# Kernel tuning notes

Measured on AMD Instinct MI355X. Metric: run time of the kernel, lower is better.

The kernel has to match this reference:

```python
import jax, jax.numpy as jnp
import numpy as np

HEADS = 16
DIM = 1024
D_K = DIM // HEADS
SEQ = 2048


def setup_inputs() -> dict:
    key = jax.random.key(0)
    ks = jax.random.split(key, 11)
    s = 1.0 / np.sqrt(DIM).astype(np.float32)
    return {
        "q": jax.random.normal(ks[0], (SEQ, DIM), jnp.float32),
        "k": jax.random.normal(ks[1], (SEQ, DIM), jnp.float32),
        "v": jax.random.normal(ks[2], (SEQ, DIM), jnp.float32),
        "Wq": jax.random.normal(ks[3], (DIM, DIM), jnp.float32) * s,
        "bq": jax.random.normal(ks[4], (DIM,), jnp.float32) * 0.01,
        "Wk": jax.random.normal(ks[5], (DIM, DIM), jnp.float32) * s,
        "bk": jax.random.normal(ks[6], (DIM,), jnp.float32) * 0.01,
        "Wv": jax.random.normal(ks[7], (DIM, DIM), jnp.float32) * s,
        "bv": jax.random.normal(ks[8], (DIM,), jnp.float32) * 0.01,
        "Wo": jax.random.normal(ks[9], (DIM, DIM), jnp.float32) * s,
        "bo": jax.random.normal(ks[10], (DIM,), jnp.float32) * 0.01,
    }


def reference(q, k, v, Wq, bq, Wk, bk, Wv, bv, Wo, bo):
    S = q.shape[0]
    # torch Linear: x @ W.T + b; view to (1, S, H, d_k) then transpose to (1, H, S, d_k)
    def proj(x, W, b):
        return (x @ W.T + b).reshape(1, S, HEADS, D_K).transpose(0, 2, 1, 3)

    qh = proj(q, Wq, bq)  # (1, H, S, d)
    kh = proj(k, Wk, bk)
    vh = proj(v, Wv, bv)

    scale = 1.0 / np.sqrt(D_K).astype(np.float32)
    scores = jnp.einsum("bhqd,bhkd->bhqk", qh, kh) * scale  # (1, H, S, S)
    # NOTE: source applies softmax over dim=1 == the HEADS axis (faithful quirk)
    attn = jax.nn.softmax(scores, axis=1)
    ctx = jnp.einsum("bhqk,bhkd->bhqd", attn, vh)  # (1, H, S, d)
    concat = ctx.transpose(0, 2, 1, 3).reshape(1, S, DIM)
    return concat @ Wo.T + bo
```

## Files before the change

kernel.cpp:

```cpp
#include <hip/hip_runtime.h>
#include <hip/hip_fp16.h>


typedef _Float16 f16;
typedef _Float16 f16x4 __attribute__((ext_vector_type(4)));
typedef _Float16 f16x8 __attribute__((ext_vector_type(8)));
typedef float    f32x4 __attribute__((ext_vector_type(4)));

#define S_LEN 2048
#define DIM   1024
#define NH    16
#define DK    64
#define EXP2K 0.1803368801111244f

#define MFMA(a, b, c) __builtin_amdgcn_mfma_f32_16x16x32_f16(a, b, c, 0, 0, 0)

#define VM_WAIT0   asm volatile("s_waitcnt vmcnt(0)" ::: "memory")
#define WG_BARRIER asm volatile("s_barrier" ::: "memory")

typedef __attribute__((address_space(1))) void g_void;
typedef __attribute__((address_space(3))) void l_void;

static __device__ __forceinline__ void gload_lds16(const void* g, void* l) {
  __builtin_amdgcn_global_load_lds((g_void*)g, (l_void*)l, 16, 0, 0);
}

static __device__ __forceinline__ float exp_s(float s) {
  return __builtin_amdgcn_exp2f(s * EXP2K);
}

__global__ __launch_bounds__(256) void cvt_all(
    const float* __restrict__ q, const float* __restrict__ k, const float* __restrict__ v,
    const float* __restrict__ Wq, const float* __restrict__ Wk, const float* __restrict__ Wv,
    const float* __restrict__ Wo, f16* __restrict__ qh, f16* __restrict__ kh,
    f16* __restrict__ vh, f16* __restrict__ wqh, f16* __restrict__ wkh,
    f16* __restrict__ wvh, f16* __restrict__ woh) {
  const size_t M = 1048576;
  const int seg = blockIdx.y;
  const float* src;
  f16* dst;
  switch (seg) {
    case 0: src = q;      dst = qh;      break;
    case 1: src = q + M;  dst = qh + M;  break;
    case 2: src = k;      dst = kh;      break;
    case 3: src = k + M;  dst = kh + M;  break;
    case 4: src = v;      dst = vh;      break;
    case 5: src = v + M;  dst = vh + M;  break;
    case 6: src = Wq;     dst = wqh;     break;
    case 7: src = Wk;     dst = wkh;     break;
    case 8: src = Wv;     dst = wvh;     break;
    default: src = Wo;    dst = woh;     break;
  }
  int i = blockIdx.x * 256 + threadIdx.x;
  float4 vv = ((const float4*)src)[i];
  f16x4 o = {(f16)vv.x, (f16)vv.y, (f16)vv.z, (f16)vv.w};
  ((f16x4*)dst)[i] = o;
}

__global__ __launch_bounds__(256) void sum_halves(const f16* __restrict__ a,
                                                  const f16* __restrict__ b,
                                                  f16* __restrict__ o) {
  int i = blockIdx.x * 256 + threadIdx.x;
  f16x8 x = ((const f16x8*)a)[i];
  f16x8 y = ((const f16x8*)b)[i];
  f16x8 r;
#pragma unroll
  for (int j = 0; j < 8; j++) r[j] = (f16)((float)x[j] + (float)y[j]);
  ((f16x8*)o)[i] = r;
}

static __device__ __forceinline__ void gemm32_core(const f16* __restrict__ X,
                                                   const f16* __restrict__ W,
                                                   int k0, int k1, int bm, int bn,
                                                   f16* As, f16* Bs,
                                                   f32x4 (&acc)[4][2]) {
  const int tid = threadIdx.x;
  const int wv = tid >> 6;
  const int lane = tid & 63;
  const int qd = lane >> 4;
  const int l16 = lane & 15;
  const int wm = (wv & 1) * 64;
  const int wn = (wv >> 1) * 32;
  const int lr4 = lane >> 2, lc4 = lane & 3;

  const f16* gA = X + (size_t)(bm + wv * 32 + lr4) * DIM + k0 + lc4 * 8;
  const f16* gB = W + (size_t)(bn + wv * 16 + lr4) * DIM + k0 + lc4 * 8;
  const int np = (k1 - k0) >> 5;

  gload_lds16(gA, As + (wv * 32) * 32);
  gload_lds16(gA + 16 * DIM, As + (wv * 32 + 16) * 32);
  gload_lds16(gB, Bs + (wv * 16) * 32);

#pragma unroll 2
  for (int t = 0; t < np; t++) {
    const int buf = t & 1;
    VM_WAIT0;
    WG_BARRIER;
    if (t + 1 < np) {
      const f16* gA1 = gA + (t + 1) * 32;
      const f16* gB1 = gB + (t + 1) * 32;
      f16* dA = As + (buf ^ 1) * (128 * 32);
      f16* dB = Bs + (buf ^ 1) * (64 * 32);
      gload_lds16(gA1, dA + (wv * 32) * 32);
      gload_lds16(gA1 + 16 * DIM, dA + (wv * 32 + 16) * 32);
      gload_lds16(gB1, dB + (wv * 16) * 32);
    }
    const f16* A = As + buf * (128 * 32);
    const f16* B = Bs + buf * (64 * 32);
    f16x8 bf[2];
#pragma unroll
    for (int ni = 0; ni < 2; ni++)
      bf[ni] = *(const f16x8*)&B[(wn + ni * 16 + l16) * 32 + qd * 8];
#pragma unroll
    for (int mi = 0; mi < 4; mi++) {
      f16x8 af = *(const f16x8*)&A[(wm + mi * 16 + l16) * 32 + qd * 8];
#pragma unroll
      for (int ni = 0; ni < 2; ni++)
        acc[mi][ni] = MFMA(af, bf[ni], acc[mi][ni]);
    }
  }
}

__global__ __launch_bounds__(256) void gemm_qkv(
    const f16* __restrict__ X0, const f16* __restrict__ X1, const f16* __restrict__ X2,
    const f16* __restrict__ W0, const f16* __restrict__ W1, const f16* __restrict__ W2,
    const float* __restrict__ b0, const float* __restrict__ b1, const float* __restrict__ b2,
    f16* __restrict__ o0, f16* __restrict__ o1, f16* __restrict__ o2) {
  __shared__ __align__(16) f16 As[2 * 128 * 32];
  __shared__ __align__(16) f16 Bs[2 * 64 * 32];
  const int z = blockIdx.z;
  const f16* X = z == 0 ? X0 : z == 1 ? X1 : X2;
  const f16* W = z == 0 ? W0 : z == 1 ? W1 : W2;
  const float* bias = z == 0 ? b0 : z == 1 ? b1 : b2;
  f16* outh = z == 0 ? o0 : z == 1 ? o1 : o2;

  const int bm = blockIdx.y * 128, bn = blockIdx.x * 64;
  f32x4 acc[4][2];
#pragma unroll
  for (int a = 0; a < 4; a++)
#pragma unroll
    for (int b = 0; b < 2; b++) acc[a][b] = (f32x4){0.f, 0.f, 0.f, 0.f};

  gemm32_core(X, W, 0, DIM, bm, bn, As, Bs, acc);

  const int tid = threadIdx.x;
  const int wv = tid >> 6, lane = tid & 63;
  const int qd = lane >> 4, l16 = lane & 15;
  const int wm = (wv & 1) * 64, wn = (wv >> 1) * 32;
#pragma unroll
  for (int mi = 0; mi < 4; mi++) {
#pragma unroll
    for (int ni = 0; ni < 2; ni++) {
      const int gm = bm + wm + mi * 16 + qd * 4;
      const int gn = bn + wn + ni * 16 + l16;
      const float bs = bias[gn];
      if (z == 2) {
        f16x4 o = {(f16)(acc[mi][ni][0] + bs), (f16)(acc[mi][ni][1] + bs),
                   (f16)(acc[mi][ni][2] + bs), (f16)(acc[mi][ni][3] + bs)};
        const int pj = (gm & ~31) + ((gm >> 2) & 3) * 8 + ((gm >> 4) & 1) * 4;
        *(f16x4*)&outh[(size_t)gn * S_LEN + pj] = o;
      } else {
#pragma unroll
        for (int r = 0; r < 4; r++)
          outh[(size_t)(gm + r) * DIM + gn] = (f16)(acc[mi][ni][r] + bs);
      }
    }
  }
}

__global__ __launch_bounds__(256) void gemm_out(const f16* __restrict__ X,
                                                const f16* __restrict__ W,
                                                const float* __restrict__ bias,
                                                float* __restrict__ outf) {
  __shared__ __align__(16) f16 As[2 * 64 * 32];
  __shared__ __align__(16) f16 Bs[2 * 64 * 32];
  const int tid = threadIdx.x;
  const int wv = tid >> 6;
  const int lane = tid & 63;
  const int qd = lane >> 4;
  const int l16 = lane & 15;
  const int wm = (wv & 1) * 32;
  const int wn = (wv >> 1) * 32;
  const int lr4 = lane >> 2, lc4 = lane & 3;
  const int bm = blockIdx.y * 64, bn = blockIdx.x * 64;

  const f16* gA = X + (size_t)(bm + wv * 16 + lr4) * DIM + lc4 * 8;
  const f16* gB = W + (size_t)(bn + wv * 16 + lr4) * DIM + lc4 * 8;

  f32x4 acc[2][2];
#pragma unroll
  for (int a = 0; a < 2; a++)
#pragma unroll
    for (int b = 0; b < 2; b++) acc[a][b] = (f32x4){0.f, 0.f, 0.f, 0.f};

  gload_lds16(gA, As + (wv * 16) * 32);
  gload_lds16(gB, Bs + (wv * 16) * 32);

#pragma unroll 2
  for (int t = 0; t < 32; t++) {
    const int buf = t & 1;
    VM_WAIT0;
    WG_BARRIER;
    if (t + 1 < 32) {
      gload_lds16(gA + (t + 1) * 32, As + (buf ^ 1) * (64 * 32) + (wv * 16) * 32);
      gload_lds16(gB + (t + 1) * 32, Bs + (buf ^ 1) * (64 * 32) + (wv * 16) * 32);
    }
    const f16* A = As + buf * (64 * 32);
    const f16* B = Bs + buf * (64 * 32);
    f16x8 bf[2];
#pragma unroll
    for (int ni = 0; ni < 2; ni++)
      bf[ni] = *(const f16x8*)&B[(wn + ni * 16 + l16) * 32 + qd * 8];
#pragma unroll
    for (int mi = 0; mi < 2; mi++) {
      f16x8 af = *(const f16x8*)&A[(wm + mi * 16 + l16) * 32 + qd * 8];
#pragma unroll
      for (int ni = 0; ni < 2; ni++)
        acc[mi][ni] = MFMA(af, bf[ni], acc[mi][ni]);
    }
  }

#pragma unroll
  for (int mi = 0; mi < 2; mi++) {
#pragma unroll
    for (int ni = 0; ni < 2; ni++) {
      const int gm = bm + wm + mi * 16 + qd * 4;
      const int gn = bn + wn + ni * 16 + l16;
      const float bs = bias[gn];
#pragma unroll
      for (int r = 0; r < 4; r++)
        outf[(size_t)(gm + r) * DIM + gn] = acc[mi][ni][r] + bs;
    }
  }
}

__global__ __launch_bounds__(256) void attn_denom(const f16* __restrict__ Qp,
                                                  const f16* __restrict__ Kp,
                                                  f16* __restrict__ IDn) {
  __shared__ __align__(16) f16 Qs[2][2][64 * 32];
  __shared__ __align__(16) f16 Ks[2][2][64 * 32];
  const int tid = threadIdx.x;
  const int wv = tid >> 6;
  const int lane = tid & 63;
  const int qd = lane >> 4;
  const int l16 = lane & 15;
  const int wm = (wv & 1) * 32, wn = (wv >> 1) * 32;
  const int flat = blockIdx.x + (blockIdx.y << 5);
  const int nf = ((flat & 7) << 7) + (flat >> 3);
  const int bi = (nf >> 5) * 64, bj = (nf & 31) * 64;
  const int lr4 = lane >> 2, lc4 = lane & 3;
  const int kkw = wv & 1;
  const int q0 = (wv >> 1) * 2;
  const int ssw = (lc4 ^ ((lr4 >> 1) & 3)) * 8;
  const int rsw = (qd ^ ((l16 >> 1) & 3)) * 8;

  f32x4 dsum[2][2];
#pragma unroll
  for (int a = 0; a < 2; a++)
#pragma unroll
    for (int b = 0; b < 2; b++) dsum[a][b] = (f32x4){0.f, 0.f, 0.f, 0.f};

  {
    const f16* gq = Qp + (size_t)(bi + q0 * 16 + lr4) * DIM + kkw * 32 + ssw;
    const f16* gk = Kp + (size_t)(bj + q0 * 16 + lr4) * DIM + kkw * 32 + ssw;
#pragma unroll
    for (int t = 0; t < 2; t++) {
      gload_lds16(gq + (size_t)t * 16 * DIM, &Qs[0][kkw][(q0 + t) * 16 * 32]);
      gload_lds16(gk + (size_t)t * 16 * DIM, &Ks[0][kkw][(q0 + t) * 16 * 32]);
    }
  }

#pragma unroll 2
  for (int h = 0; h < NH; h++) {
    const int buf = h & 1;
    VM_WAIT0;
    WG_BARRIER;
    if (h + 1 < NH) {
      const f16* gq = Qp + (size_t)(bi + q0 * 16 + lr4) * DIM + (h + 1) * DK + kkw * 32 + ssw;
      const f16* gk = Kp + (size_t)(bj + q0 * 16 + lr4) * DIM + (h + 1) * DK + kkw * 32 + ssw;
#pragma unroll
      for (int t = 0; t < 2; t++) {
        gload_lds16(gq + (size_t)t * 16 * DIM, &Qs[buf ^ 1][kkw][(q0 + t) * 16 * 32]);
        gload_lds16(gk + (size_t)t * 16 * DIM, &Ks[buf ^ 1][kkw][(q0 + t) * 16 * 32]);
      }
    }

#pragma unroll
    for (int mi = 0; mi < 2; mi++) {
      f16x8 af0 = *(const f16x8*)&Qs[buf][0][(wm + mi * 16 + l16) * 32 + rsw];
      f16x8 af1 = *(const f16x8*)&Qs[buf][1][(wm + mi * 16 + l16) * 32 + rsw];
#pragma unroll
      for (int ni = 0; ni < 2; ni++) {
        f16x8 bf0 = *(const f16x8*)&Ks[buf][0][(wn + ni * 16 + l16) * 32 + rsw];
        f16x8 bf1 = *(const f16x8*)&Ks[buf][1][(wn + ni * 16 + l16) * 32 + rsw];
        f32x4 s = {0.f, 0.f, 0.f, 0.f};
        s = MFMA(af0, bf0, s);
        s = MFMA(af1, bf1, s);
#pragma unroll
        for (int r = 0; r < 4; r++) dsum[mi][ni][r] += exp_s(s[r]);
      }
    }
  }
#pragma unroll
  for (int mi = 0; mi < 2; mi++)
#pragma unroll
    for (int ni = 0; ni < 2; ni++)
#pragma unroll
      for (int r = 0; r < 4; r++) {
        const int gi = bi + wm + mi * 16 + qd * 4 + r;
        const int gj = bj + wn + ni * 16 + l16;
        const int pj = (gj & ~31) + ((gj >> 2) & 3) * 8 + ((gj >> 4) & 1) * 4 + (gj & 3);
        IDn[(size_t)gi * S_LEN + pj] = (f16)(1.f / dsum[mi][ni][r]);
      }
}

__global__ __launch_bounds__(256, 4) void attn_ctx(const f16* __restrict__ Qp,
                                                   const f16* __restrict__ Kp,
                                                   const f16* __restrict__ Vt,
                                                   const f16* __restrict__ IDn,
                                                   f16* __restrict__ C0,
                                                   f16* __restrict__ C1) {
  __shared__ __align__(16) f16 Ks[2][2][64 * 32];
  __shared__ __align__(16) f16 Vs[2][64 * 64];
  const int tid = threadIdx.x;
  const int wv = tid >> 6;
  const int lane = tid & 63;
  const int qd = lane >> 4;
  const int l16 = lane & 15;
  const int flat = blockIdx.x + (blockIdx.y << 5) + (blockIdx.z << 9);
  const int nf = ((flat & 7) << 7) + (flat >> 3);
  const int h = (nf >> 5) & 15;
  const int iw = (nf & 31) * 64 + wv * 16;
  const int z = nf >> 9;
  const int jb = z * 1024;
  f16* Cz = z == 0 ? C0 : C1;
  const int lr4 = lane >> 2, lc4 = lane & 3;
  const int lr8 = lane >> 3, lc8 = lane & 7;
  const int kkw = wv & 1;
  const int rhw = wv >> 1;
  const int ssw = (lc4 ^ ((lr4 >> 1) & 3)) * 8;
  const int rsw = (qd ^ ((l16 >> 1) & 3)) * 8;
  const int l7 = l16 & 7;

  f16x8 aq[2];
#pragma unroll
  for (int kk = 0; kk < 2; kk++)
    aq[kk] = *(const f16x8*)(Qp + (size_t)(iw + l16) * DIM + h * DK + kk * 32 + qd * 8);

  f32x4 acc[4];
#pragma unroll
  for (int b = 0; b < 4; b++) acc[b] = (f32x4){0.f, 0.f, 0.f, 0.f};

  f16x8 idn[2][2];

  auto issue = [&](int tt, int pb) {
    const int j1 = jb + tt * 64;
    const f16* gk = Kp + (size_t)(j1 + rhw * 16 + lr4) * DIM + h * DK + kkw * 32 + ssw;
    gload_lds16(gk, &Ks[pb][kkw][(rhw * 16) * 32]);
    gload_lds16(gk + (size_t)32 * DIM, &Ks[pb][kkw][(rhw * 16 + 32) * 32]);
    const f16* gv = Vt + (size_t)(h * DK + wv * 16 + lr8) * S_LEN + j1 + (lc8 ^ lr8) * 8;
    gload_lds16(gv, &Vs[pb][(wv * 16) * 64]);
    gload_lds16(gv + (size_t)8 * S_LEN, &Vs[pb][(wv * 16 + 8) * 64]);
#pragma unroll
    for (int js = 0; js < 2; js++)
      idn[pb][js] = *(const f16x8*)(IDn + (size_t)(iw + l16) * S_LEN + j1 + js * 32 + qd * 8);
  };

  issue(0, 0);

#pragma unroll 2
  for (int t = 0; t < 16; t++) {
    const int buf = t & 1;
    VM_WAIT0;
    WG_BARRIER;
    if (t + 1 < 16) issue(t + 1, buf ^ 1);

    f16x8 pa[2];
#pragma unroll
    for (int js = 0; js < 2; js++) {
      f16x8 bk0[2], bk1[2];
#pragma unroll
      for (int kk = 0; kk < 2; kk++) {
        bk0[kk] = *(const f16x8*)&Ks[buf][kk][((js * 2) * 16 + l16) * 32 + rsw];
        bk1[kk] = *(const f16x8*)&Ks[buf][kk][((js * 2 + 1) * 16 + l16) * 32 + rsw];
      }
      f32x4 st0 = {0.f, 0.f, 0.f, 0.f};
      f32x4 st1 = {0.f, 0.f, 0.f, 0.f};
      st0 = MFMA(bk0[0], aq[0], st0);
      st0 = MFMA(bk0[1], aq[1], st0);
      st1 = MFMA(bk1[0], aq[0], st1);
      st1 = MFMA(bk1[1], aq[1], st1);
      f16x8 p;
#pragma unroll
      for (int r = 0; r < 4; r++) p[r] = (f16)(exp_s(st0[r]) * (float)idn[buf][js][r]);
#pragma unroll
      for (int r = 0; r < 4; r++) p[4 + r] = (f16)(exp_s(st1[r]) * (float)idn[buf][js][4 + r]);
      pa[js] = p;
    }

#pragma unroll
    for (int js = 0; js < 2; js++) {
#pragma unroll
      for (int nd = 0; nd < 4; nd++) {
        f16x8 bv = *(const f16x8*)&Vs[buf][(nd * 16 + l16) * 64 +
                                          (((js * 4 + qd) ^ l7) * 8)];
        acc[nd] = MFMA(pa[js], bv, acc[nd]);
      }
    }
  }

#pragma unroll
  for (int nd = 0; nd < 4; nd++)
#pragma unroll
    for (int r = 0; r < 4; r++)
      Cz[(size_t)(iw + qd * 4 + r) * DIM + h * DK + nd * 16 + l16] = (f16)acc[nd][r];
}

extern "C" void kernel_launch(void* const* d_in, const int* in_sizes, int n_in,
                              void* d_out, int out_size, void* d_ws, size_t ws_size,
                              hipStream_t stream) {
  const float* q  = (const float*)d_in[0];
  const float* k  = (const float*)d_in[1];
  const float* v  = (const float*)d_in[2];
  const float* Wq = (const float*)d_in[3];
  const float* bq = (const float*)d_in[4];
  const float* Wk = (const float*)d_in[5];
  const float* bk = (const float*)d_in[6];
  const float* Wv = (const float*)d_in[7];
  const float* bv = (const float*)d_in[8];
  const float* Wo = (const float*)d_in[9];
  const float* bo = (const float*)d_in[10];
  float* out = (float*)d_out;

  f16* w = (f16*)d_ws;
  f16* qh  = w;
  f16* kh  = qh + (size_t)S_LEN * DIM;
  f16* vh  = kh + (size_t)S_LEN * DIM;
  f16* wqh = vh + (size_t)S_LEN * DIM;
  f16* wkh = wqh + (size_t)DIM * DIM;
  f16* wvh = wkh + (size_t)DIM * DIM;
  f16* woh = wvh + (size_t)DIM * DIM;
  f16* Qp  = woh + (size_t)DIM * DIM;
  f16* Kp  = Qp + (size_t)S_LEN * DIM;
  f16* Vt  = Kp + (size_t)S_LEN * DIM;
  f16* IDn = qh;
  f16* C0  = vh;
  f16* C1  = wqh;
  f16* Ct  = qh;

  dim3 b256(256);
  cvt_all<<<dim3(1024, 10), b256, 0, stream>>>(q, k, v, Wq, Wk, Wv, Wo,
                                               qh, kh, vh, wqh, wkh, wvh, woh);

  gemm_qkv<<<dim3(DIM / 64, S_LEN / 128, 3), b256, 0, stream>>>(
      qh, kh, vh, wqh, wkh, wvh, bq, bk, bv, Qp, Kp, Vt);

  attn_denom<<<dim3(S_LEN / 64, S_LEN / 64), b256, 0, stream>>>(Qp, Kp, IDn);
  attn_ctx<<<dim3(S_LEN / 64, NH, 2), b256, 0, stream>>>(Qp, Kp, Vt, IDn, C0, C1);

  const int n8 = S_LEN * DIM / 8;
  sum_halves<<<n8 / 256, b256, 0, stream>>>(C0, C1, Ct);

  gemm_out<<<dim3(DIM / 64, S_LEN / 64), b256, 0, stream>>>(Ct, woh, bo, out);
}
```

Baseline: 205.2 us.

## Fuse context half-sum into output GEMM and use K=64 swizzled LDS tiles

Removes the separate sum_halves kernel: the output GEMM now loads both context halves into registers, adds them, and writes the sum to LDS itself. Both GEMMs move from K-step 32 to K-step 64 with an XOR-swizzled LDS layout to avoid bank conflicts, halving the number of barrier iterations. Costs are double the LDS per block, which may lower occupancy, and register-staged A loads in gemm_out instead of direct global-to-LDS copies.

```diff
diff --git a/kernel.cpp b/kernel.cpp
--- a/kernel.cpp
+++ b/kernel.cpp
@@ -16,6 +16,7 @@
 #define MFMA(a, b, c) __builtin_amdgcn_mfma_f32_16x16x32_f16(a, b, c, 0, 0, 0)
 
 #define VM_WAIT0   asm volatile("s_waitcnt vmcnt(0)" ::: "memory")
+#define LGKM_WAIT0 asm volatile("s_waitcnt lgkmcnt(0)" ::: "memory")
 #define WG_BARRIER asm volatile("s_barrier" ::: "memory")
 
 typedef __attribute__((address_space(1))) void g_void;
@@ -57,21 +58,9 @@
   ((f16x4*)dst)[i] = o;
 }
 
-__global__ __launch_bounds__(256) void sum_halves(const f16* __restrict__ a,
-                                                  const f16* __restrict__ b,
-                                                  f16* __restrict__ o) {
-  int i = blockIdx.x * 256 + threadIdx.x;
-  f16x8 x = ((const f16x8*)a)[i];
-  f16x8 y = ((const f16x8*)b)[i];
-  f16x8 r;
-#pragma unroll
-  for (int j = 0; j < 8; j++) r[j] = (f16)((float)x[j] + (float)y[j]);
-  ((f16x8*)o)[i] = r;
-}
-
-static __device__ __forceinline__ void gemm32_core(const f16* __restrict__ X,
+static __device__ __forceinline__ void gemm64_core(const f16* __restrict__ X,
                                                    const f16* __restrict__ W,
-                                                   int k0, int k1, int bm, int bn,
+                                                   int bm, int bn,
                                                    f16* As, f16* Bs,
                                                    f32x4 (&acc)[4][2]) {
   const int tid = threadIdx.x;
@@ -81,42 +70,46 @@
   const int l16 = lane & 15;
   const int wm = (wv & 1) * 64;
   const int wn = (wv >> 1) * 32;
-  const int lr4 = lane >> 2, lc4 = lane & 3;
-
-  const f16* gA = X + (size_t)(bm + wv * 32 + lr4) * DIM + k0 + lc4 * 8;
-  const f16* gB = W + (size_t)(bn + wv * 16 + lr4) * DIM + k0 + lc4 * 8;
-  const int np = (k1 - k0) >> 5;
-
-  gload_lds16(gA, As + (wv * 32) * 32);
-  gload_lds16(gA + 16 * DIM, As + (wv * 32 + 16) * 32);
-  gload_lds16(gB, Bs + (wv * 16) * 32);
+  const int lr8 = lane >> 3, lc8 = lane & 7;
+  const int l7 = l16 & 7;
+
+  const f16* gA = X + (size_t)(bm + wv * 32 + lr8) * DIM + (lc8 ^ lr8) * 8;
+  const f16* gB = W + (size_t)(bn + wv * 16 + lr8) * DIM + (lc8 ^ lr8) * 8;
+
+  auto issue = [&](int t, f16* dA, f16* dB) {
+#pragma unroll
+    for (int g = 0; g < 4; g++)
+      gload_lds16(gA + (size_t)(g * 8) * DIM + t * 64, dA + (wv * 32 + g * 8) * 64);
+#pragma unroll
+    for (int g = 0; g < 2; g++)
+      gload_lds16(gB + (size_t)(g * 8) * DIM + t * 64, dB + (wv * 16 + g * 8) * 64);
+  };
+
+  issue(0, As, Bs);
 
 #pragma unroll 2
-  for (int t = 0; t < np; t++) {
+  for (int t = 0; t < 16; t++) {
     const int buf = t & 1;
     VM_WAIT0;
     WG_BARRIER;
-    if (t + 1 < np) {
-      const f16* gA1 = gA + (t + 1) * 32;
-      const f16* gB1 = gB + (t + 1) * 32;
-      f16* dA = As + (buf ^ 1) * (128 * 32);
-      f16* dB = Bs + (buf ^ 1) * (64 * 32);
-      gload_lds16(gA1, dA + (wv * 32) * 32);
-      gload_lds16(gA1 + 16 * DIM, dA + (wv * 32 + 16) * 32);
-      gload_lds16(gB1, dB + (wv * 16) * 32);
-    }
-    const f16* A = As + buf * (128 * 32);
-    const f16* B = Bs + buf * (64 * 32);
-    f16x8 bf[2];
-#pragma unroll
-    for (int ni = 0; ni < 2; ni++)
-      bf[ni] = *(const f16x8*)&B[(wn + ni * 16 + l16) * 32 + qd * 8];
-#pragma unroll
-    for (int mi = 0; mi < 4; mi++) {
-      f16x8 af = *(const f16x8*)&A[(wm + mi * 16 + l16) * 32 + qd * 8];
+    if (t + 1 < 16)
+      issue(t + 1, As + (buf ^ 1) * (128 * 64), Bs + (buf ^ 1) * (64 * 64));
+    const f16* A = As + buf * (128 * 64);
+    const f16* B = Bs + buf * (64 * 64);
+#pragma unroll
+    for (int kk = 0; kk < 2; kk++) {
+      const int slot = ((kk * 4 + qd) ^ l7) * 8;
+      f16x8 bf[2];
 #pragma unroll
       for (int ni = 0; ni < 2; ni++)
-        acc[mi][ni] = MFMA(af, bf[ni], acc[mi][ni]);
+        bf[ni] = *(const f16x8*)&B[(wn + ni * 16 + l16) * 64 + slot];
+#pragma unroll
+      for (int mi = 0; mi < 4; mi++) {
+        f16x8 af = *(const f16x8*)&A[(wm + mi * 16 + l16) * 64 + slot];
+#pragma unroll
+        for (int ni = 0; ni < 2; ni++)
+          acc[mi][ni] = MFMA(af, bf[ni], acc[mi][ni]);
+      }
     }
   }
 }
@@ -126,8 +119,8 @@
     const f16* __restrict__ W0, const f16* __restrict__ W1, const f16* __restrict__ W2,
     const float* __restrict__ b0, const float* __restrict__ b1, const float* __restrict__ b2,
     f16* __restrict__ o0, f16* __restrict__ o1, f16* __restrict__ o2) {
-  __shared__ __align__(16) f16 As[2 * 128 * 32];
-  __shared__ __align__(16) f16 Bs[2 * 64 * 32];
+  __shared__ __align__(16) f16 As[2 * 128 * 64];
+  __shared__ __align__(16) f16 Bs[2 * 64 * 64];
   const int z = blockIdx.z;
   const f16* X = z == 0 ? X0 : z == 1 ? X1 : X2;
   const f16* W = z == 0 ? W0 : z == 1 ? W1 : W2;
@@ -141,7 +134,7 @@
 #pragma unroll
     for (int b = 0; b < 2; b++) acc[a][b] = (f32x4){0.f, 0.f, 0.f, 0.f};
 
-  gemm32_core(X, W, 0, DIM, bm, bn, As, Bs, acc);
+  gemm64_core(X, W, bm, bn, As, Bs, acc);
 
   const int tid = threadIdx.x;
   const int wv = tid >> 6, lane = tid & 63;
@@ -168,12 +161,13 @@
   }
 }
 
-__global__ __launch_bounds__(256) void gemm_out(const f16* __restrict__ X,
+__global__ __launch_bounds__(256) void gemm_out(const f16* __restrict__ C0,
+                                                const f16* __restrict__ C1,
                                                 const f16* __restrict__ W,
                                                 const float* __restrict__ bias,
                                                 float* __restrict__ outf) {
-  __shared__ __align__(16) f16 As[2 * 64 * 32];
-  __shared__ __align__(16) f16 Bs[2 * 64 * 32];
+  __shared__ __align__(16) f16 As[2 * 64 * 64];
+  __shared__ __align__(16) f16 Bs[2 * 64 * 64];
   const int tid = threadIdx.x;
   const int wv = tid >> 6;
   const int lane = tid & 63;
@@ -181,11 +175,27 @@
   const int l16 = lane & 15;
   const int wm = (wv & 1) * 32;
   const int wn = (wv >> 1) * 32;
-  const int lr4 = lane >> 2, lc4 = lane & 3;
+  const int lr8 = lane >> 3, lc8 = lane & 7;
+  const int l7 = l16 & 7;
   const int bm = blockIdx.y * 64, bn = blockIdx.x * 64;
 
-  const f16* gA = X + (size_t)(bm + wv * 16 + lr4) * DIM + lc4 * 8;
-  const f16* gB = W + (size_t)(bn + wv * 16 + lr4) * DIM + lc4 * 8;
+  const f16* gA0 = C0 + (size_t)(bm + wv * 16 + lr8) * DIM + lc8 * 8;
+  const f16* gA1 = C1 + (size_t)(bm + wv * 16 + lr8) * DIM + lc8 * 8;
+  const f16* gB  = W + (size_t)(bn + wv * 16 + lr8) * DIM + (lc8 ^ lr8) * 8;
+
+  f16x8 a0[2], a1[2];
+  auto issueA = [&](int t) {
+#pragma unroll
+    for (int g = 0; g < 2; g++) {
+      a0[g] = *(const f16x8*)(gA0 + (size_t)(g * 8) * DIM + t * 64);
+      a1[g] = *(const f16x8*)(gA1 + (size_t)(g * 8) * DIM + t * 64);
+    }
+  };
+  auto issueB = [&](int t, f16* dB) {
+#pragma unroll
+    for (int g = 0; g < 2; g++)
+      gload_lds16(gB + (size_t)(g * 8) * DIM + t * 64, dB + (wv * 16 + g * 8) * 64);
+  };
 
   f32x4 acc[2][2];
 #pragma unroll
@@ -193,30 +203,44 @@
 #pragma unroll
     for (int b = 0; b < 2; b++) acc[a][b] = (f32x4){0.f, 0.f, 0.f, 0.f};
 
-  gload_lds16(gA, As + (wv * 16) * 32);
-  gload_lds16(gB, Bs + (wv * 16) * 32);
+  issueA(0);
+  issueB(0, Bs);
 
 #pragma unroll 2
-  for (int t = 0; t < 32; t++) {
+  for (int t = 0; t < 16; t++) {
     const int buf = t & 1;
     VM_WAIT0;
+    f16* Ab = As + buf * (64 * 64);
+#pragma unroll
+    for (int g = 0; g < 2; g++) {
+      f16x8 s;
+#pragma unroll
+      for (int j = 0; j < 8; j++) s[j] = (f16)((float)a0[g][j] + (float)a1[g][j]);
+      *(f16x8*)&Ab[(wv * 16 + g * 8 + lr8) * 64 + (lc8 ^ lr8) * 8] = s;
+    }
+    LGKM_WAIT0;
     WG_BARRIER;
-    if (t + 1 < 32) {
-      gload_lds16(gA + (t + 1) * 32, As + (buf ^ 1) * (64 * 32) + (wv * 16) * 32);
-      gload_lds16(gB + (t + 1) * 32, Bs + (buf ^ 1) * (64 * 32) + (wv * 16) * 32);
-    }
-    const f16* A = As + buf * (64 * 32);
-    const f16* B = Bs + buf * (64 * 32);
-    f16x8 bf[2];
-#pragma unroll
-    for (int ni = 0; ni < 2; ni++)
-      bf[ni] = *(const f16x8*)&B[(wn + ni * 16 + l16) * 32 + qd * 8];
-#pragma unroll
-    for (int mi = 0; mi < 2; mi++) {
-      f16x8 af = *(const f16x8*)&A[(wm + mi * 16 + l16) * 32 + qd * 8];
+    if (t + 1 < 16) {
+      issueA(t + 1);
+      issueB(t + 1, Bs + (buf ^ 1) * (64 * 64));
+    }
+    const f16* A = Ab;
+    const f16* B = Bs + buf * (64 * 64);
+#pragma unroll
+    for (int kk = 0; kk < 2; kk++) {
+      const int slot = ((kk * 4 + qd) ^ l7) * 8;
+      f16x8 bf[2], af[2];
 #pragma unroll
       for (int ni = 0; ni < 2; ni++)
-        acc[mi][ni] = MFMA(af, bf[ni], acc[mi][ni]);
+        bf[ni] = *(const f16x8*)&B[(wn + ni * 16 + l16) * 64 + slot];
+#pragma unroll
+      for (int mi = 0; mi < 2; mi++)
+        af[mi] = *(const f16x8*)&A[(wm + mi * 16 + l16) * 64 + slot];
+#pragma unroll
+      for (int mi = 0; mi < 2; mi++)
+#pragma unroll
+        for (int ni = 0; ni < 2; ni++)
+          acc[mi][ni] = MFMA(af[mi], bf[ni], acc[mi][ni]);
     }
   }
 
@@ -446,7 +470,6 @@
   f16* IDn = qh;
   f16* C0  = vh;
   f16* C1  = wqh;
-  f16* Ct  = qh;
 
   dim3 b256(256);
   cvt_all<<<dim3(1024, 10), b256, 0, stream>>>(q, k, v, Wq, Wk, Wv, Wo,
@@ -458,8 +481,5 @@
   attn_denom<<<dim3(S_LEN / 64, S_LEN / 64), b256, 0, stream>>>(Qp, Kp, IDn);
   attn_ctx<<<dim3(S_LEN / 64, NH, 2), b256, 0, stream>>>(Qp, Kp, Vt, IDn, C0, C1);
 
-  const int n8 = S_LEN * DIM / 8;
-  sum_halves<<<n8 / 256, b256, 0, stream>>>(C0, C1, Ct);
-
-  gemm_out<<<dim3(DIM / 64, S_LEN / 64), b256, 0, stream>>>(Ct, woh, bo, out);
-}
+  gemm_out<<<dim3(DIM / 64, S_LEN / 64), b256, 0, stream>>>(C0, C1, woh, bo, out);
+}
```

New measurement: 194.8 us (median of 2 runs). 5.1% less time.
